# Kernel optimization log

Measured on AMD Instinct MI355X. Metric: run time of the kernel, lower is better.

## Reference

```python
import jax, jax.numpy as jnp
import numpy as np
from jax import lax

B, W, L, E, V, C, H, O = 16384, 5, 20, 50, 100000, 128, 4096, 50


def setup_inputs() -> dict:
    key = jax.random.key(0)
    ks = jax.random.split(key, 10)
    x = jax.random.randint(ks[0], (B, W), 1, V)
    word_id_to_chars_ids = jax.random.randint(ks[1], (V, L), 0, C)
    word_emb = jax.random.normal(ks[2], (V, E), dtype=jnp.float32) * 0.1
    word_emb = word_emb.at[0].set(0.0)  # padding_idx=0
    char_emb = jax.random.normal(ks[3], (C, E), dtype=jnp.float32) * 0.1
    char_emb = char_emb.at[0].set(0.0)  # padding_idx=0
    conv_w = jax.random.normal(ks[4], (E, E, 3), dtype=jnp.float32) * (1.0 / np.sqrt(E * 3))
    conv_b = jax.random.normal(ks[5], (E,), dtype=jnp.float32) * 0.01
    fc1_w = jax.random.normal(ks[6], (H, E * W), dtype=jnp.float32) * (1.0 / np.sqrt(E * W))
    fc1_b = jnp.zeros((H,), dtype=jnp.float32)
    fc2_w = jax.random.normal(ks[7], (O, H), dtype=jnp.float32) * (1.0 / np.sqrt(H))
    fc2_b = jnp.zeros((O,), dtype=jnp.float32)
    return {"x": x, "word_id_to_chars_ids": word_id_to_chars_ids,
            "word_emb": word_emb, "char_emb": char_emb,
            "conv_w": conv_w, "conv_b": conv_b,
            "fc1_w": fc1_w, "fc1_b": fc1_b, "fc2_w": fc2_w, "fc2_b": fc2_b}


def reference(x, word_id_to_chars_ids, word_emb, char_emb, conv_w, conv_b,
              fc1_w, fc1_b, fc2_w, fc2_b):
    # per-window char ids: [B, 5, L] -> char embeddings [B, 5, L, E]
    char_ids = word_id_to_chars_ids[x]
    ce = char_emb[char_ids]
    # conv1d over char positions: reshape to NCW = [B*5, E, L]
    ce = ce.reshape(B * W, L, E).transpose(0, 2, 1)
    conv = lax.conv_general_dilated(ce, conv_w, window_strides=(1,),
                                    padding=[(1, 1)],
                                    dimension_numbers=("NCH", "OIH", "NCH"))
    conv = conv + conv_b[None, :, None]
    # max-pool over char positions (kernel == L): [B*5, E] -> [B, 5, E]
    chars = jnp.max(conv, axis=2).reshape(B, W, E)
    words = word_emb[x]  # [B, 5, E]
    h = (words + chars).reshape(B, W * E)  # view(-1, 250)
    h = jnp.tanh(h @ fc1_w.T + fc1_b)
    logits = h @ fc2_w.T + fc2_b
    return jax.nn.softmax(logits, axis=1)
```

## Files before the change

### kernel.cpp

```cpp
#include <hip/hip_runtime.h>
#include <hip/hip_bf16.h>


typedef __attribute__((ext_vector_type(8))) short short8;
typedef __attribute__((ext_vector_type(4))) float float4v;
typedef __attribute__((ext_vector_type(4))) _Float16 half4v;

__device__ inline short bf16b(float f) {
    __hip_bfloat16 h = __float2bfloat16(f);
    return *reinterpret_cast<short*>(&h);
}
__device__ inline uint packbf2(float a, float b) {
    return (uint)(ushort)bf16b(a) | ((uint)(ushort)bf16b(b) << 16);
}
__device__ inline void gload_lds16(const void* g, void* l) {
    __builtin_amdgcn_global_load_lds(
        (const __attribute__((address_space(1))) unsigned int*)g,
        (__attribute__((address_space(3))) unsigned int*)l, 16, 0, 0);
}
__device__ inline _Float16 hmax(_Float16 a, _Float16 b) { return a > b ? a : b; }

__global__ __launch_bounds__(256) void prep_kernel(
    const float* __restrict__ fc1_w, const float* __restrict__ fc1_b,
    const float* __restrict__ fc2_w, const float* __restrict__ char_emb,
    const float* __restrict__ conv_w, short* __restrict__ wbf,
    short* __restrict__ w2bf, _Float16* __restrict__ gt4)
{
    const int bid = blockIdx.x;
    if (bid < 4096) {
        int idx = bid * 256 + threadIdx.x;
        int n = idx >> 8, k = idx & 255;
        float v = (k < 250) ? fc1_w[n * 250 + k] : (k == 250 ? fc1_b[n] : 0.f);
        int CT = n >> 4, mm = n & 15;
        int ks = k >> 5, qq = (k >> 3) & 3, j = k & 7;
        wbf[((CT * 8 + ks) * 64 + qq * 16 + mm) * 8 + j] = bf16b(v);
    } else if (bid < 5120) {
        int idx = (bid - 4096) * 256 + threadIdx.x;
        int o = idx >> 12, k = idx & 4095;
        float v = (o < 50) ? fc2_w[idx] : 0.f;
        int Ot = o >> 4, mm = o & 15;
        int kst = k >> 5, qq = (k >> 3) & 3, j = k & 7;
        w2bf[((kst * 4 + Ot) * 64 + qq * 16 + mm) * 8 + j] = bf16b(v);
    } else {
        int idx = (bid - 5120) * 256 + threadIdx.x;
        if (idx >= 19200) return;
        int c = idx / 150, rem = idx - c * 150;
        int kk = rem / 50, o = rem - kk * 50;
        const float* ce = char_emb + c * 50;
        const float* w  = conv_w + o * 150 + kk;
        float s = 0.f;
        #pragma unroll 10
        for (int i = 0; i < 50; ++i) s += ce[i] * w[i * 3];
        gt4[(c * 50 + o) * 4 + kk] = (_Float16)s;
        if (kk == 2) gt4[(c * 50 + o) * 4 + 3] = (_Float16)0.f;
    }
}

__global__ __launch_bounds__(512, 1) void fused_kernel(
    const int* __restrict__ x, const int* __restrict__ wci,
    const float* __restrict__ word_emb, const float* __restrict__ conv_b,
    const _Float16* __restrict__ gt4, const short* __restrict__ wbf,
    const short* __restrict__ w2bf, const float* __restrict__ fc2_b,
    float* __restrict__ out)
{
    __shared__ char smem[147456];
    short8* Bsv   = (short8*)smem;
    char*   hsb   = smem + 131072;
    float*  partf = (float*)smem;
    char*   gsb   = smem;
    uint*   cpackS = (uint*)(smem + 51200);
    int*    xsS    = (int*)(smem + 57600);
    char*   haS    = smem + 110080;

    const int tid  = threadIdx.x;
    const int lane = tid & 63;
    const int wv   = tid >> 6;
    const int wr = wv >> 2, wc = wv & 3;
    const int q = lane >> 4, m = lane & 15;
    const int m0 = blockIdx.x * 64;
    const int q2base = q >> 1, slot = q & 1;

    const short8* wbfv  = (const short8*)wbf;
    const short8* w2bfv = (const short8*)w2bf;

    {
        const float4* g4 = (const float4*)gt4;
        float4* s4 = (float4*)gsb;
        #pragma unroll
        for (int i = 0; i < 7; ++i) {
            int idx = i * 512 + tid;
            if (idx < 3200) s4[idx] = g4[idx];
        }
    }
    if (tid < 320) {
        const int xid = x[m0 * 5 + tid];
        xsS[tid] = xid;
        const int* crow = wci + (size_t)xid * 20;
        int cid[20];
        #pragma unroll
        for (int p = 0; p < 20; ++p) cid[p] = crow[p];
        #pragma unroll
        for (int u = 0; u < 5; ++u)
            cpackS[tid * 5 + u] = (uint)cid[u * 4] | ((uint)cid[u * 4 + 1] << 8)
                                | ((uint)cid[u * 4 + 2] << 16) | ((uint)cid[u * 4 + 3] << 24);
    }
    if (tid < 384) {
        const int s = tid / 6, j = tid - s * 6;
        const int byteoff = (s * 512 + (250 + j) * 2) ^ ((s & 7) << 4);
        *(short*)(haS + byteoff) = bf16b(j == 0 ? 1.f : 0.f);
    }
    __syncthreads();

    {
        const int oc = (lane < 50) ? lane : 49;
        const float cbias = conv_b[oc];
        const int oc8 = oc * 8;
        for (int g = 0; g < 5; ++g) {
            float werv[8];
            #pragma unroll
            for (int j = 0; j < 8; ++j) {
                const int w = (g * 8 + j) * 8 + wv;
                werv[j] = word_emb[(size_t)xsS[w] * 50 + oc];
            }
            #pragma unroll
            for (int j = 0; j < 8; ++j) {
                const int w = (g * 8 + j) * 8 + wv;
                uint cw[5];
                #pragma unroll
                for (int u = 0; u < 5; ++u) cw[u] = cpackS[w * 5 + u];
                int cb[20];
                #pragma unroll
                for (int p = 0; p < 20; ++p) {
                    const int c = (int)((cw[p >> 2] >> ((p & 3) * 8)) & 0xFF);
                    cb[p] = c * 400 + oc8;
                }
                half4v r[11];
                #pragma unroll
                for (int l = 0; l < 11; ++l) r[l] = *(const half4v*)(gsb + cb[l]);
                _Float16 mxh = r[0].y + r[1].z;
                #pragma unroll
                for (int l = 1; l < 10; ++l) {
                    _Float16 s = r[l].y + r[l - 1].x + r[l + 1].z;
                    mxh = hmax(mxh, s);
                }
                const half4v r9 = r[9], r10 = r[10];
                half4v qv[9];
                #pragma unroll
                for (int l = 0; l < 9; ++l) qv[l] = *(const half4v*)(gsb + cb[11 + l]);
                mxh = hmax(mxh, (_Float16)(r10.y + r9.x + qv[0].z));
                mxh = hmax(mxh, (_Float16)(qv[0].y + r10.x + qv[1].z));
                #pragma unroll
                for (int l = 12; l < 19; ++l) {
                    _Float16 s = qv[l - 11].y + qv[l - 12].x + qv[l - 10].z;
                    mxh = hmax(mxh, s);
                }
                mxh = hmax(mxh, (_Float16)(qv[8].y + qv[7].x));

                if (lane < 50) {
                    const int s = w / 5, wp = w - s * 5;
                    const int byteoff = (s * 512 + (wp * 50 + oc) * 2) ^ ((s & 7) << 4);
                    *(short*)(haS + byteoff) = bf16b((float)mxh + cbias + werv[j]);
                }
            }
        }
    }
    __syncthreads();

    #pragma unroll
    for (int i = 0; i < 8; ++i)
        gload_lds16(wbfv + i * 512 + tid, Bsv + i * 512 + tid);

    short8 av[2][8];
    #pragma unroll
    for (int mt = 0; mt < 2; ++mt)
        #pragma unroll
        for (int ks = 0; ks < 8; ++ks) {
            const int r = wr * 32 + mt * 16 + m;
            const int byteoff = (r * 512 + ks * 64 + q * 16) ^ ((r & 7) << 4);
            av[mt][ks] = *(const short8*)(haS + byteoff);
        }
    #pragma unroll
    for (int mt = 0; mt < 2; ++mt)
        #pragma unroll
        for (int ks = 0; ks < 8; ++ks)
            asm volatile("" : "+v"(av[mt][ks]));
    __syncthreads();

    float4v acc2[2][4] = {};

    #pragma unroll 4
    for (int chg = 0; chg < 32; ++chg) {
        const int buf = chg & 1;

        short8 b2[4];
        #pragma unroll
        for (int Ot = 0; Ot < 4; ++Ot)
            b2[Ot] = w2bfv[(size_t)((chg * 4 + wc) * 4 + Ot) * 64 + lane];

        #pragma unroll
        for (int i = 0; i < 8; ++i)
            gload_lds16(wbfv + (size_t)(chg + 1) * 4096 + i * 512 + tid,
                        Bsv + (buf ^ 1) * 4096 + i * 512 + tid);

        float4v acc[2][2] = {};
        #pragma unroll
        for (int ks = 0; ks < 8; ++ks) {
            short8 bv[2];
            #pragma unroll
            for (int nt = 0; nt < 2; ++nt)
                bv[nt] = Bsv[buf * 4096 + ((wc * 2 + nt) * 8 + ks) * 64 + lane];
            #pragma unroll
            for (int mt = 0; mt < 2; ++mt)
                #pragma unroll
                for (int nt = 0; nt < 2; ++nt)
                    acc[mt][nt] = __builtin_amdgcn_mfma_f32_16x16x32_bf16(
                        bv[nt], av[mt][ks], acc[mt][nt], 0, 0, 0);
        }

        #pragma unroll
        for (int mt = 0; mt < 2; ++mt) {
            const int frag = (wr * 2 + mt) * 4 + wc;
            #pragma unroll
            for (int nt = 0; nt < 2; ++nt) {
                float tv[4];
                #pragma unroll
                for (int r = 0; r < 4; ++r) {
                    float rc = __builtin_amdgcn_rcpf(
                        __expf(2.f * acc[mt][nt][r]) + 1.f);
                    tv[r] = fmaf(-2.f, rc, 1.f);
                }
                const int q2 = nt * 2 + q2base;
                const uint p0 = packbf2(tv[0], tv[1]);
                const uint p1 = packbf2(tv[2], tv[3]);
                *(uint2*)(hsb + ((frag * 64 + q2 * 16 + m) * 16 + slot * 8))
                    = make_uint2(p0, p1);
            }
        }

        {
            short8 a2[2];
            #pragma unroll
            for (int mt = 0; mt < 2; ++mt)
                a2[mt] = *(const short8*)(hsb
                    + (((wr * 2 + mt) * 4 + wc) * 64 + lane) * 16);
            #pragma unroll
            for (int mt = 0; mt < 2; ++mt)
                #pragma unroll
                for (int Ot = 0; Ot < 4; ++Ot)
                    acc2[mt][Ot] = __builtin_amdgcn_mfma_f32_16x16x32_bf16(
                        a2[mt], b2[Ot], acc2[mt][Ot], 0, 0, 0);
        }

        __syncthreads();
    }

    #pragma unroll
    for (int mt = 0; mt < 2; ++mt)
        #pragma unroll
        for (int Ot = 0; Ot < 4; ++Ot)
            #pragma unroll
            for (int r = 0; r < 4; ++r)
                partf[(size_t)wc * 4096
                      + ((wr * 2 + mt) * 16 + q * 4 + r) * 64 + Ot * 16 + m]
                    = acc2[mt][Ot][r];
    __syncthreads();

    #pragma unroll
    for (int t = 0; t < 8; ++t) {
        int idx = t * 512 + tid;
        int col = idx & 63;
        float lg = partf[idx] + partf[4096 + idx]
                 + partf[8192 + idx] + partf[12288 + idx];
        partf[idx] = (col < 50) ? lg + fc2_b[col] : -1e30f;
    }
    __syncthreads();

    #pragma unroll
    for (int rr = 0; rr < 8; ++rr) {
        const int row = wv * 8 + rr;
        float v = partf[row * 64 + lane];
        float mx = v;
        #pragma unroll
        for (int off = 32; off > 0; off >>= 1) mx = fmaxf(mx, __shfl_xor(mx, off));
        float e = __expf(v - mx);
        float s = e;
        #pragma unroll
        for (int off = 32; off > 0; off >>= 1) s += __shfl_xor(s, off);
        if (lane < 50)
            out[(size_t)(m0 + row) * 50 + lane] = e / s;
    }
}

extern "C" void kernel_launch(void* const* d_in, const int* in_sizes, int n_in,
                              void* d_out, int out_size, void* d_ws, size_t ws_size,
                              hipStream_t stream) {
    const int*   x        = (const int*)  d_in[0];
    const int*   wci      = (const int*)  d_in[1];
    const float* word_emb = (const float*)d_in[2];
    const float* char_emb = (const float*)d_in[3];
    const float* conv_w   = (const float*)d_in[4];
    const float* conv_b   = (const float*)d_in[5];
    const float* fc1_w    = (const float*)d_in[6];
    const float* fc1_b    = (const float*)d_in[7];
    const float* fc2_w    = (const float*)d_in[8];
    const float* fc2_b    = (const float*)d_in[9];
    float* out = (float*)d_out;

    char* ws = (char*)d_ws;
    short* wbf  = (short*)(ws + ((size_t)8  << 20));
    short* w2bf = (short*)(ws + ((size_t)10 << 20));
    _Float16* gt4 = (_Float16*)(ws + ((size_t)11 << 20));

    prep_kernel<<<5195, 256, 0, stream>>>(fc1_w, fc1_b, fc2_w, char_emb,
                                          conv_w, wbf, w2bf, gt4);
    fused_kernel<<<256, 512, 0, stream>>>(x, wci, word_emb, conv_b, gt4,
                                          wbf, w2bf, fc2_b, out);
}
```

Baseline: 171.8 us.

## Halve block tile to 32 rows with 256 threads, two blocks per CU

Restructures the fused kernel so each block handles 32 batch rows with 4 waves instead of 64 rows with 8 waves. LDS use is cut to about 70KB so two blocks can be resident per CU, and the grid doubles to 512 blocks. The aim is better latency hiding and overlap between the gather/conv phase and the MFMA phase. In exchange, fc1 weight tiles are streamed into LDS twice as many times overall, which adds L2 traffic and lowers reuse per load.

```diff
diff --git a/kernel.cpp b/kernel.cpp
--- a/kernel.cpp
+++ b/kernel.cpp
@@ -56,28 +56,28 @@
     }
 }
 
-__global__ __launch_bounds__(512, 1) void fused_kernel(
+__global__ __launch_bounds__(256, 2) void fused_kernel(
     const int* __restrict__ x, const int* __restrict__ wci,
     const float* __restrict__ word_emb, const float* __restrict__ conv_b,
     const _Float16* __restrict__ gt4, const short* __restrict__ wbf,
     const short* __restrict__ w2bf, const float* __restrict__ fc2_b,
     float* __restrict__ out)
 {
-    __shared__ char smem[147456];
+    __shared__ char smem[71680];
     short8* Bsv   = (short8*)smem;
-    char*   hsb   = smem + 131072;
+    char*   hsb   = smem + 65536;
     float*  partf = (float*)smem;
     char*   gsb   = smem;
     uint*   cpackS = (uint*)(smem + 51200);
-    int*    xsS    = (int*)(smem + 57600);
-    char*   haS    = smem + 110080;
+    int*    xsS    = (int*)(smem + 54400);
+    char*   haS    = smem + 55040;
 
     const int tid  = threadIdx.x;
     const int lane = tid & 63;
     const int wv   = tid >> 6;
-    const int wr = wv >> 2, wc = wv & 3;
+    const int wr = wv >> 1, wc = wv & 1;
     const int q = lane >> 4, m = lane & 15;
-    const int m0 = blockIdx.x * 64;
+    const int m0 = blockIdx.x * 32;
     const int q2base = q >> 1, slot = q & 1;
 
     const short8* wbfv  = (const short8*)wbf;
@@ -87,12 +87,12 @@
         const float4* g4 = (const float4*)gt4;
         float4* s4 = (float4*)gsb;
         #pragma unroll
-        for (int i = 0; i < 7; ++i) {
-            int idx = i * 512 + tid;
+        for (int i = 0; i < 13; ++i) {
+            int idx = i * 256 + tid;
             if (idx < 3200) s4[idx] = g4[idx];
         }
     }
-    if (tid < 320) {
+    if (tid < 160) {
         const int xid = x[m0 * 5 + tid];
         xsS[tid] = xid;
         const int* crow = wci + (size_t)xid * 20;
@@ -104,7 +104,7 @@
             cpackS[tid * 5 + u] = (uint)cid[u * 4] | ((uint)cid[u * 4 + 1] << 8)
                                 | ((uint)cid[u * 4 + 2] << 16) | ((uint)cid[u * 4 + 3] << 24);
     }
-    if (tid < 384) {
+    if (tid < 192) {
         const int s = tid / 6, j = tid - s * 6;
         const int byteoff = (s * 512 + (250 + j) * 2) ^ ((s & 7) << 4);
         *(short*)(haS + byteoff) = bf16b(j == 0 ? 1.f : 0.f);
@@ -119,12 +119,12 @@
             float werv[8];
             #pragma unroll
             for (int j = 0; j < 8; ++j) {
-                const int w = (g * 8 + j) * 8 + wv;
+                const int w = (g * 8 + j) * 4 + wv;
                 werv[j] = word_emb[(size_t)xsS[w] * 50 + oc];
             }
             #pragma unroll
             for (int j = 0; j < 8; ++j) {
-                const int w = (g * 8 + j) * 8 + wv;
+                const int w = (g * 8 + j) * 4 + wv;
                 uint cw[5];
                 #pragma unroll
                 for (int u = 0; u < 5; ++u) cw[u] = cpackS[w * 5 + u];
@@ -168,65 +168,58 @@
 
     #pragma unroll
     for (int i = 0; i < 8; ++i)
-        gload_lds16(wbfv + i * 512 + tid, Bsv + i * 512 + tid);
-
-    short8 av[2][8];
-    #pragma unroll
-    for (int mt = 0; mt < 2; ++mt)
-        #pragma unroll
-        for (int ks = 0; ks < 8; ++ks) {
-            const int r = wr * 32 + mt * 16 + m;
-            const int byteoff = (r * 512 + ks * 64 + q * 16) ^ ((r & 7) << 4);
-            av[mt][ks] = *(const short8*)(haS + byteoff);
-        }
-    #pragma unroll
-    for (int mt = 0; mt < 2; ++mt)
-        #pragma unroll
-        for (int ks = 0; ks < 8; ++ks)
-            asm volatile("" : "+v"(av[mt][ks]));
-    __syncthreads();
-
-    float4v acc2[2][4] = {};
+        gload_lds16(wbfv + i * 256 + tid, Bsv + i * 256 + tid);
+
+    short8 av[8];
+    #pragma unroll
+    for (int ks = 0; ks < 8; ++ks) {
+        const int r = wr * 16 + m;
+        const int byteoff = (r * 512 + ks * 64 + q * 16) ^ ((r & 7) << 4);
+        av[ks] = *(const short8*)(haS + byteoff);
+    }
+    #pragma unroll
+    for (int ks = 0; ks < 8; ++ks)
+        asm volatile("" : "+v"(av[ks]));
+    __syncthreads();
+
+    float4v acc2[4] = {};
 
     #pragma unroll 4
-    for (int chg = 0; chg < 32; ++chg) {
+    for (int chg = 0; chg < 64; ++chg) {
         const int buf = chg & 1;
 
         short8 b2[4];
         #pragma unroll
         for (int Ot = 0; Ot < 4; ++Ot)
-            b2[Ot] = w2bfv[(size_t)((chg * 4 + wc) * 4 + Ot) * 64 + lane];
+            b2[Ot] = w2bfv[(size_t)((chg * 2 + wc) * 4 + Ot) * 64 + lane];
 
         #pragma unroll
         for (int i = 0; i < 8; ++i)
-            gload_lds16(wbfv + (size_t)(chg + 1) * 4096 + i * 512 + tid,
-                        Bsv + (buf ^ 1) * 4096 + i * 512 + tid);
-
-        float4v acc[2][2] = {};
+            gload_lds16(wbfv + (size_t)(chg + 1) * 2048 + i * 256 + tid,
+                        Bsv + (buf ^ 1) * 2048 + i * 256 + tid);
+
+        float4v acc[2] = {};
         #pragma unroll
         for (int ks = 0; ks < 8; ++ks) {
             short8 bv[2];
             #pragma unroll
             for (int nt = 0; nt < 2; ++nt)
-                bv[nt] = Bsv[buf * 4096 + ((wc * 2 + nt) * 8 + ks) * 64 + lane];
-            #pragma unroll
-            for (int mt = 0; mt < 2; ++mt)
-                #pragma unroll
-                for (int nt = 0; nt < 2; ++nt)
-                    acc[mt][nt] = __builtin_amdgcn_mfma_f32_16x16x32_bf16(
-                        bv[nt], av[mt][ks], acc[mt][nt], 0, 0, 0);
-        }
-
-        #pragma unroll
-        for (int mt = 0; mt < 2; ++mt) {
-            const int frag = (wr * 2 + mt) * 4 + wc;
+                bv[nt] = Bsv[buf * 2048 + ((wc * 2 + nt) * 8 + ks) * 64 + lane];
+            #pragma unroll
+            for (int nt = 0; nt < 2; ++nt)
+                acc[nt] = __builtin_amdgcn_mfma_f32_16x16x32_bf16(
+                    bv[nt], av[ks], acc[nt], 0, 0, 0);
+        }
+
+        {
+            const int frag = wr * 2 + wc;
             #pragma unroll
             for (int nt = 0; nt < 2; ++nt) {
                 float tv[4];
                 #pragma unroll
                 for (int r = 0; r < 4; ++r) {
                     float rc = __builtin_amdgcn_rcpf(
-                        __expf(2.f * acc[mt][nt][r]) + 1.f);
+                        __expf(2.f * acc[nt][r]) + 1.f);
                     tv[r] = fmaf(-2.f, rc, 1.f);
                 }
                 const int q2 = nt * 2 + q2base;
@@ -238,39 +231,30 @@
         }
 
         {
-            short8 a2[2];
-            #pragma unroll
-            for (int mt = 0; mt < 2; ++mt)
-                a2[mt] = *(const short8*)(hsb
-                    + (((wr * 2 + mt) * 4 + wc) * 64 + lane) * 16);
-            #pragma unroll
-            for (int mt = 0; mt < 2; ++mt)
-                #pragma unroll
-                for (int Ot = 0; Ot < 4; ++Ot)
-                    acc2[mt][Ot] = __builtin_amdgcn_mfma_f32_16x16x32_bf16(
-                        a2[mt], b2[Ot], acc2[mt][Ot], 0, 0, 0);
+            short8 a2 = *(const short8*)(hsb
+                + ((wr * 2 + wc) * 64 + lane) * 16);
+            #pragma unroll
+            for (int Ot = 0; Ot < 4; ++Ot)
+                acc2[Ot] = __builtin_amdgcn_mfma_f32_16x16x32_bf16(
+                    a2, b2[Ot], acc2[Ot], 0, 0, 0);
         }
 
         __syncthreads();
     }
 
     #pragma unroll
-    for (int mt = 0; mt < 2; ++mt)
-        #pragma unroll
-        for (int Ot = 0; Ot < 4; ++Ot)
-            #pragma unroll
-            for (int r = 0; r < 4; ++r)
-                partf[(size_t)wc * 4096
-                      + ((wr * 2 + mt) * 16 + q * 4 + r) * 64 + Ot * 16 + m]
-                    = acc2[mt][Ot][r];
+    for (int Ot = 0; Ot < 4; ++Ot)
+        #pragma unroll
+        for (int r = 0; r < 4; ++r)
+            partf[wc * 2048 + (wr * 16 + q * 4 + r) * 64 + Ot * 16 + m]
+                = acc2[Ot][r];
     __syncthreads();
 
     #pragma unroll
     for (int t = 0; t < 8; ++t) {
-        int idx = t * 512 + tid;
+        int idx = t * 256 + tid;
         int col = idx & 63;
-        float lg = partf[idx] + partf[4096 + idx]
-                 + partf[8192 + idx] + partf[12288 + idx];
+        float lg = partf[idx] + partf[2048 + idx];
         partf[idx] = (col < 50) ? lg + fc2_b[col] : -1e30f;
     }
     __syncthreads();
@@ -313,6 +297,6 @@
 
     prep_kernel<<<5195, 256, 0, stream>>>(fc1_w, fc1_b, fc2_w, char_emb,
                                           conv_w, wbf, w2bf, gt4);
-    fused_kernel<<<256, 512, 0, stream>>>(x, wci, word_emb, conv_b, gt4,
+    fused_kernel<<<512, 256, 0, stream>>>(x, wci, word_emb, conv_b, gt4,
                                           wbf, w2bf, fc2_b, out);
 }
```

New measurement: 191.9 us. 1.12x slower.
